# Performance work log

Measured on AMD Instinct MI355X. Metric: run time of the kernel, lower is better.

## Reference

```python
import jax, jax.numpy as jnp
import numpy as np

EMBED = 1024
N_HEAD = 16
D_HID = EMBED // N_HEAD
R_FF = 4
D_FF = EMBED * R_FF
LN_EPS = 1e-5


def layer_norm(x, gamma, beta):
    mu = jnp.mean(x, axis=-1, keepdims=True)
    var = jnp.var(x, axis=-1, keepdims=True)
    return (x - mu) * jax.lax.rsqrt(var + LN_EPS) * gamma + beta


def setup_inputs() -> dict:
    key = jax.random.key(0)
    ks = jax.random.split(key, 10)
    B, S = 4, 2048
    # torch nn.Linear stores weight as [out, in]; y = x @ W.T
    def xavier(k, shape):
        fan_out, fan_in = shape
        lim = np.sqrt(6.0 / (fan_in + fan_out))
        return jax.random.uniform(k, shape, jnp.float32, -lim, lim)
    return {
        "x": jax.random.normal(ks[0], (B, S, EMBED), jnp.float32),
        "Wq": xavier(ks[1], (EMBED, EMBED)),
        "Wk": xavier(ks[2], (EMBED, EMBED)),
        "Wv": xavier(ks[3], (EMBED, EMBED)),
        "Wo": xavier(ks[4], (EMBED, EMBED)),
        "bo": jnp.zeros((EMBED,), jnp.float32),
        "ln1_g": jnp.ones((EMBED,), jnp.float32),
        "ln1_b": jnp.zeros((EMBED,), jnp.float32),
        "ln2_g": jnp.ones((EMBED,), jnp.float32),
        "ln2_b": jnp.zeros((EMBED,), jnp.float32),
        "W1": jax.random.normal(ks[5], (D_FF, EMBED), jnp.float32) * np.sqrt(2.0 / EMBED),
        "b1": jnp.zeros((D_FF,), jnp.float32),
        "W2": xavier(ks[6], (EMBED, D_FF)),
        "b2": jnp.zeros((EMBED,), jnp.float32),
    }


def reference(x, Wq, Wk, Wv, Wo, bo, ln1_g, ln1_b, ln2_g, ln2_b, W1, b1, W2, b2):
    B, S, E = x.shape
    scaling = 1.0 / np.sqrt(D_HID)
    # --- attention (pre-LN), dropout = identity (eval) ---
    xn = layer_norm(x, ln1_g, ln1_b)
    q = (xn @ Wq.T).reshape(B, S, N_HEAD, D_HID) * scaling
    k = (xn @ Wk.T).reshape(B, S, N_HEAD, D_HID)
    v = (xn @ Wv.T).reshape(B, S, N_HEAD, D_HID)
    scores = jnp.einsum("bqhd,bkhd->bhqk", q, k)
    attn = jax.nn.softmax(scores, axis=-1)
    out = jnp.einsum("bhqk,bkhd->bqhd", attn, v).reshape(B, S, E)
    out = out @ Wo.T + bo
    x = x + out
    # --- feed-forward (pre-LN) ---
    xn = layer_norm(x, ln2_g, ln2_b)
    h = jax.nn.relu(xn @ W1.T + b1)
    x = x + (h @ W2.T + b2)
    return x
```

## Files before the change

kernel.cpp:

```cpp
#include <hip/hip_runtime.h>
#include <hip/hip_bf16.h>
#include <cstdint>


typedef __attribute__((ext_vector_type(8))) short bf16x8;
typedef __attribute__((ext_vector_type(4))) float f32x4;

#define LDSAS __attribute__((address_space(3)))
#define GLBAS __attribute__((address_space(1)))

#define CQK 0.18033688011112044f

union APU { unsigned u[4]; bf16x8 v; };

__device__ __forceinline__ unsigned short f2bf(float f) {
  union { float f; unsigned u; } c; c.f = f;
  unsigned u = c.u + 0x7fffu + ((c.u >> 16) & 1u);
  return (unsigned short)(u >> 16);
}

__device__ __forceinline__ unsigned pk2(float a, float b) {
  __hip_bfloat162 h = __float22bfloat162_rn(make_float2(a, b));
  union { __hip_bfloat162 h; unsigned u; } c; c.h = h; return c.u;
}

__device__ __forceinline__ void async16(const unsigned short* g, unsigned short* l) {
  __builtin_amdgcn_global_load_lds((const GLBAS unsigned int*)g,
                                   (LDSAS unsigned int*)l, 16, 0, 0);
}

__global__ void cvt_all(const float* __restrict__ q, const float* __restrict__ k,
                        const float* __restrict__ v, const float* __restrict__ o,
                        const float* __restrict__ w1, const float* __restrict__ w2,
                        unsigned short* __restrict__ wsb) {
  const long i = (long)blockIdx.x * 256 + threadIdx.x;
  const float* src; unsigned short* dst; long off;
  if (i < 1048576) {
    const long seg = i >> 18, o4 = i & 262143;
    src = (seg == 0) ? q : (seg == 1) ? k : (seg == 2) ? v : o;
    dst = wsb + ((seg == 3) ? 3145728L : seg * 1048576L);
    off = o4;
  } else if (i < 2097152) {
    src = w1; dst = wsb + 4194304; off = i - 1048576;
  } else {
    src = w2; dst = wsb + 8388608; off = i - 2097152;
  }
  const float4 vv = ((const float4*)src)[off];
  ushort4 r;
  r.x = f2bf(vv.x); r.y = f2bf(vv.y); r.z = f2bf(vv.z); r.w = f2bf(vv.w);
  ((ushort4*)dst)[off] = r;
}

__global__ void ln_fwd(const float* __restrict__ x, const float* __restrict__ g,
                       const float* __restrict__ bb, unsigned short* __restrict__ outp) {
  const int row = blockIdx.x, tid = threadIdx.x;
  const float4 v = ((const float4*)(x + (long)row * 1024))[tid];
  float s  = v.x + v.y + v.z + v.w;
  float sq = v.x * v.x + v.y * v.y + v.z * v.z + v.w * v.w;
#pragma unroll
  for (int off = 1; off < 64; off <<= 1) {
    s  += __shfl_xor(s, off);
    sq += __shfl_xor(sq, off);
  }
  __shared__ float red[8];
  const int wv = tid >> 6, lane = tid & 63;
  if (lane == 0) { red[wv] = s; red[4 + wv] = sq; }
  __syncthreads();
  s  = red[0] + red[1] + red[2] + red[3];
  sq = red[4] + red[5] + red[6] + red[7];
  const float mu  = s * (1.f / 1024.f);
  const float var = sq * (1.f / 1024.f) - mu * mu;
  const float rstd = rsqrtf(var + 1e-5f);
  const float4 gv = ((const float4*)g)[tid];
  const float4 bv = ((const float4*)bb)[tid];
  ushort4 o;
  o.x = f2bf((v.x - mu) * rstd * gv.x + bv.x);
  o.y = f2bf((v.y - mu) * rstd * gv.y + bv.y);
  o.z = f2bf((v.z - mu) * rstd * gv.z + bv.z);
  o.w = f2bf((v.w - mu) * rstd * gv.w + bv.w);
  ((ushort4*)(outp + (long)row * 1024))[tid] = o;
}

template <int EPI>
__launch_bounds__(256, 3)
__global__ void gemm_bt(const unsigned short* __restrict__ A,
                        const unsigned short* __restrict__ B,
                        void* __restrict__ Cout,
                        const float* __restrict__ bias,
                        const float* __restrict__ res,
                        unsigned short* __restrict__ vt4,
                        int M, int N, int K) {
  __shared__ __align__(16) unsigned short As[128 * 64];
  __shared__ __align__(16) unsigned short Bs[128 * 64];
  const int tid  = threadIdx.x;
  const int lane = tid & 63;
  const int wvu  = __builtin_amdgcn_readfirstlane(tid >> 6);
  const int quad = lane >> 4, l16 = lane & 15;
  const int wm = wvu >> 1, wn = wvu & 1;

  const int gx = gridDim.x;
  const int id = blockIdx.y * gx + blockIdx.x;
  const int xcd = id & 7, slot = id >> 3;
  const int by = xcd * 8 + (slot & 7);
  const int bx = slot >> 3;
  const long m0 = (long)by * 128, n0 = (long)bx * 128;

  f32x4 acc[4][4];
#pragma unroll
  for (int i = 0; i < 4; i++)
#pragma unroll
    for (int j = 0; j < 4; j++) acc[i][j] = (f32x4){0.f, 0.f, 0.f, 0.f};

  const int rxA = l16 & 7;
  const int c0A = quad ^ rxA;
  int srow[4], sgc[4];
#pragma unroll
  for (int j = 0; j < 4; ++j) {
    const int s = wvu * 256 + j * 64 + lane;
    srow[j] = s >> 3;
    sgc[j] = ((s & 7) ^ (srow[j] & 7)) * 8;
  }

  for (int k0 = 0; k0 < K; k0 += 64) {
    __syncthreads();
#pragma unroll
    for (int j = 0; j < 4; ++j) {
      const int db = (wvu * 256 + j * 64) * 8;
      async16(A + (m0 + srow[j]) * K + k0 + sgc[j], As + db);
      async16(B + (n0 + srow[j]) * K + k0 + sgc[j], Bs + db);
    }
    __syncthreads();

#pragma unroll
    for (int kc = 0; kc < 2; ++kc) {
      const int ch = (c0A ^ (kc * 4)) * 8;
      bf16x8 af[4], bfr[4];
#pragma unroll
      for (int t = 0; t < 4; ++t) {
        af[t]  = *(const bf16x8*)(As + (wm * 64 + t * 16 + l16) * 64 + ch);
        bfr[t] = *(const bf16x8*)(Bs + (wn * 64 + t * 16 + l16) * 64 + ch);
      }
#pragma unroll
      for (int mt = 0; mt < 4; ++mt)
#pragma unroll
        for (int nt = 0; nt < 4; ++nt)
          acc[mt][nt] = __builtin_amdgcn_mfma_f32_16x16x32_bf16(af[mt], bfr[nt],
                                                                acc[mt][nt], 0, 0, 0);
    }
  }

  if (EPI == 3) {
#pragma unroll
    for (int nt = 0; nt < 4; ++nt) {
      const long col = n0 + wn * 64 + nt * 16 + l16;
      if (col < 2048) {
        const float scl = (col < 1024) ? CQK : 1.0f;
#pragma unroll
        for (int mt = 0; mt < 4; ++mt)
#pragma unroll
          for (int r = 0; r < 4; ++r) {
            const long row = m0 + wm * 64 + mt * 16 + quad * 4 + r;
            ((unsigned short*)Cout)[row * (long)N + col] = f2bf(acc[mt][nt][r] * scl);
          }
      } else {
        const int hd = (int)(col - 2048);
        const int h = hd >> 6, d = hd & 63;
#pragma unroll
        for (int mt = 0; mt < 4; ++mt) {
          const long row = m0 + wm * 64 + mt * 16 + quad * 4;
          const int b_ = (int)(row >> 11);
          const int kv = (int)(row & 2047);
          const int t_ = kv >> 6;
          const int sk = kv & 63;
          const int kvp4 = (sk & 32) | ((sk & 16) >> 2) | ((sk & 8) << 1) | ((sk & 4) << 1);
          const int kk = kvp4 >> 3, half = (kvp4 >> 2) & 1;
          const int cc = d * 8 + ((kk + d) & 7);
          const int u = cc * 2 + half;
          ushort4 o;
          o.x = f2bf(acc[mt][nt][0]);
          o.y = f2bf(acc[mt][nt][1]);
          o.z = f2bf(acc[mt][nt][2]);
          o.w = f2bf(acc[mt][nt][3]);
          *(ushort4*)(vt4 + ((long)((b_ * 16 + h) * 32 + t_)) * 4096 + u * 4) = o;
        }
      }
    }
  } else {
#pragma unroll
    for (int nt = 0; nt < 4; ++nt) {
      const long col = n0 + wn * 64 + nt * 16 + l16;
      float bv = 0.f;
      if (EPI == 1 || EPI == 2) bv = bias[col];
#pragma unroll
      for (int mt = 0; mt < 4; ++mt) {
#pragma unroll
        for (int r = 0; r < 4; ++r) {
          const long row = m0 + wm * 64 + mt * 16 + quad * 4 + r;
          const long idx = row * (long)N + col;
          float v = acc[mt][nt][r];
          if (EPI == 0) {
            ((unsigned short*)Cout)[idx] = f2bf(v);
          } else if (EPI == 1) {
            ((float*)Cout)[idx] = v + bv + res[idx];
          } else {
            v += bv;
            ((unsigned short*)Cout)[idx] = f2bf(v > 0.f ? v : 0.f);
          }
        }
      }
    }
  }
}

#define W2_LDA(AF, BUF, H)                                                      \
  do {                                                                          \
    const unsigned short* _p = As + ((BUF) * 2 + (H)) * 4096;                   \
    _Pragma("unroll") for (int _m = 0; _m < 2; ++_m) {                          \
      AF[_m][0] = *(const bf16x8*)(_p + (_m * 32 + rA) * 64 + chk0);            \
      AF[_m][1] = *(const bf16x8*)(_p + (_m * 32 + rA) * 64 + chk1);            \
    }                                                                           \
  } while (0)

#define W2_LDB(BF, BUF, H)                                                      \
  do {                                                                          \
    const unsigned short* _p = Bs + ((BUF) * 2 + (H)) * 8192;                   \
    _Pragma("unroll") for (int _n = 0; _n < 2; ++_n) {                          \
      BF[_n][0] = *(const bf16x8*)(_p + (_n * 64 + rB) * 64 + chk0);            \
      BF[_n][1] = *(const bf16x8*)(_p + (_n * 64 + rB) * 64 + chk1);            \
    }                                                                           \
  } while (0)

#define W2_MFMA(AH, BH, AF, BF)                                                 \
  do {                                                                          \
    _Pragma("unroll") for (int _m = 0; _m < 2; ++_m)                            \
    _Pragma("unroll") for (int _n = 0; _n < 2; ++_n) {                          \
      acc[(AH) * 2 + _m][(BH) * 2 + _n] =                                       \
          __builtin_amdgcn_mfma_f32_16x16x32_bf16(                              \
              AF[_m][0], BF[_n][0], acc[(AH) * 2 + _m][(BH) * 2 + _n], 0, 0, 0);\
      acc[(AH) * 2 + _m][(BH) * 2 + _n] =                                       \
          __builtin_amdgcn_mfma_f32_16x16x32_bf16(                              \
              AF[_m][1], BF[_n][1], acc[(AH) * 2 + _m][(BH) * 2 + _n], 0, 0, 0);\
    }                                                                           \
  } while (0)

#define PH_MID()                                                                \
  __builtin_amdgcn_s_barrier();                                                 \
  asm volatile("s_waitcnt lgkmcnt(0)" ::: "memory");                            \
  __builtin_amdgcn_sched_barrier(0);                                            \
  __builtin_amdgcn_s_setprio(1)

#define PH_END()                                                                \
  __builtin_amdgcn_s_setprio(0);                                                \
  __builtin_amdgcn_sched_barrier(0);                                            \
  __builtin_amdgcn_s_barrier();                                                 \
  __builtin_amdgcn_sched_barrier(0)

__launch_bounds__(512, 2)
__global__ void gemm_w2(const unsigned short* __restrict__ A,
                        const unsigned short* __restrict__ B,
                        float* __restrict__ Cout,
                        const float* __restrict__ bias,
                        const float* __restrict__ res,
                        int M, int N, int K) {
  extern __shared__ __align__(16) unsigned short lds[];
  unsigned short* As = lds;
  unsigned short* Bs = lds + 16384;

  const int tid  = threadIdx.x;
  const int lane = tid & 63;
  const int wv   = __builtin_amdgcn_readfirstlane(tid >> 6);
  const int quad = lane >> 4, l16 = lane & 15;
  const int wm = wv >> 2, wn = wv & 3;

  const int id = blockIdx.x;
  const int xcd = id & 7, slot = id >> 3;
  const int by = xcd * 8 + (slot & 7);
  const int bx = slot >> 3;
  const long m0 = (long)by * 128, n0 = (long)bx * 256;

  const int s0 = wv * 64 + lane;
  const int r0 = s0 >> 3;
  const int c0 = (s0 ^ r0) & 7;
  const int s1 = 512 + s0;
  const int r1 = s1 >> 3;
  const int c1 = (s1 ^ r1) & 7;
  const long rt0 = (long)r0 * K + c0 * 8;
  const long rt1 = (long)r1 * K + c1 * 8;
  const unsigned short* Ab = A + m0 * K;
  const unsigned short* Bb = B + n0 * K;

  const int rA = wm * 16 + l16;
  const int rB = wn * 16 + l16;
  const int chk0 = (quad ^ (l16 & 7)) * 8;
  const int chk1 = chk0 ^ 32;

  f32x4 acc[4][4];
#pragma unroll
  for (int a_ = 0; a_ < 4; ++a_)
#pragma unroll
    for (int b_ = 0; b_ < 4; ++b_) acc[a_][b_] = (f32x4){0.f, 0.f, 0.f, 0.f};

  auto stgA = [&](int b, int h, long kk) {
    const unsigned short* s = Ab + (long)h * 64 * K + kk;
    async16(s + rt0, As + (b * 2 + h) * 4096 + wv * 512);
  };
  auto stgB = [&](int b, int h, long kk) {
    const unsigned short* s = Bb + (long)h * 128 * K + kk;
    unsigned short* d = Bs + (b * 2 + h) * 8192 + wv * 512;
    async16(s + rt0, d);
    async16(s + rt1, d + 4096);
  };

  stgA(0, 0, 0); stgB(0, 1, 0); stgA(0, 1, 0); stgB(0, 0, 0);
  stgA(1, 0, 64); stgB(1, 1, 64); stgA(1, 1, 64);
  asm volatile("s_waitcnt vmcnt(4)" ::: "memory");
  __builtin_amdgcn_s_barrier();
  __builtin_amdgcn_sched_barrier(0);

  const int NI = K >> 7;
  for (int it = 0; it < NI; ++it) {
    const long kt  = (long)it * 128;
    const long ku  = kt + 64;
    const long kt2 = kt + 128;
    const long kt3 = kt + 192;
    const bool more = (it + 1 < NI);

    {
      bf16x8 a0[2][2], a1[2][2], b0[2][2], b1[2][2];
      W2_LDA(a0, 0, 0); W2_LDB(b0, 0, 0);
      stgB(1, 0, ku);
      PH_MID();
      W2_MFMA(0, 0, a0, b0);
      PH_END();
      W2_LDB(b1, 0, 1);
      if (more) stgA(0, 0, kt2);
      PH_MID();
      W2_MFMA(0, 1, a0, b1);
      PH_END();
      W2_LDA(a1, 0, 1);
      if (more) stgB(0, 1, kt2);
      PH_MID();
      W2_MFMA(1, 1, a1, b1);
      PH_END();
      W2_LDB(b0, 0, 0);
      if (more) stgA(0, 1, kt2);
      PH_MID();
      W2_MFMA(1, 0, a1, b0);
      __builtin_amdgcn_s_setprio(0);
      __builtin_amdgcn_sched_barrier(0);
      if (more) { asm volatile("s_waitcnt vmcnt(4)" ::: "memory"); }
      else      { asm volatile("s_waitcnt vmcnt(0)" ::: "memory"); }
      __builtin_amdgcn_s_barrier();
      __builtin_amdgcn_sched_barrier(0);
    }
    {
      bf16x8 a0[2][2], a1[2][2], b0[2][2], b1[2][2];
      W2_LDA(a0, 1, 0); W2_LDB(b0, 1, 0);
      if (more) stgB(0, 0, kt2);
      PH_MID();
      W2_MFMA(0, 0, a0, b0);
      PH_END();
      W2_LDB(b1, 1, 1);
      if (more) stgA(1, 0, kt3);
      PH_MID();
      W2_MFMA(0, 1, a0, b1);
      PH_END();
      W2_LDA(a1, 1, 1);
      if (more) stgB(1, 1, kt3);
      PH_MID();
      W2_MFMA(1, 1, a1, b1);
      PH_END();
      W2_LDB(b0, 1, 0);
      if (more) stgA(1, 1, kt3);
      PH_MID();
      W2_MFMA(1, 0, a1, b0);
      __builtin_amdgcn_s_setprio(0);
      __builtin_amdgcn_sched_barrier(0);
      if (more) { asm volatile("s_waitcnt vmcnt(4)" ::: "memory"); }
      __builtin_amdgcn_s_barrier();
      __builtin_amdgcn_sched_barrier(0);
    }
  }

#pragma unroll
  for (int nt = 0; nt < 4; ++nt) {
    const long col = n0 + nt * 64 + wn * 16 + l16;
    const float bv = bias[col];
#pragma unroll
    for (int mt = 0; mt < 4; ++mt) {
#pragma unroll
      for (int r = 0; r < 4; ++r) {
        const long row = m0 + mt * 32 + wm * 16 + quad * 4 + r;
        const long idx = row * (long)N + col;
        Cout[idx] = acc[mt][nt][r] + bv + res[idx];
      }
    }
  }
}

__launch_bounds__(256, 4)
__global__ void attn_fwd(const unsigned short* __restrict__ qkv,
                         const unsigned short* __restrict__ vt,
                         unsigned short* __restrict__ outp) {
  __shared__ __align__(16) unsigned short lds[20480];

  const int tid = threadIdx.x;
  const int lane = tid & 63;
  const int wv = __builtin_amdgcn_readfirstlane(tid >> 6);
  const int quad = lane >> 4, l16 = lane & 15;

  const int id = blockIdx.y * 16 + blockIdx.x;
  const int xcd = id & 7, slot = id >> 3;
  const int bh = xcd * 8 + (slot >> 4);
  const int qt = slot & 15;
  const int b = bh >> 4, h = bh & 15;
  const long rowbase = (long)b * 2048;
  const int hoff = h * 64;

  const int rot0 = (quad + l16) & 7;
  const int rot1 = rot0 ^ 4;

  bf16x8 bq[2][2];
#pragma unroll
  for (int s = 0; s < 2; ++s) {
    const long qrow = rowbase + qt * 128 + wv * 32 + s * 16 + l16;
    const unsigned short* qp = qkv + qrow * 3072 + hoff;
    bq[s][0] = *(const bf16x8*)(qp + quad * 8);
    bq[s][1] = *(const bf16x8*)(qp + (quad ^ 4) * 8);
  }
  __builtin_amdgcn_sched_barrier(0);

  const int c0 = wv * 64 + lane;
  const int r0 = c0 >> 3;
  const int ks = ((c0 & 7) - r0) & 7;
  const unsigned short* kptr = qkv + (rowbase + r0) * 3072 + 1024 + hoff + ks * 8;
  const unsigned short* vptr = vt + (long)bh * 131072 + (long)c0 * 8;

  auto stage = [&](int t) {
    unsigned short* kdst = lds + ((t & 1) << 12) + wv * 512;
    unsigned short* vdst = lds + 8192 + ((t % 3) << 12) + wv * 512;
    const unsigned short* kp = kptr + (long)t * 64 * 3072;
    const unsigned short* vp = vptr + (long)t * 4096;
#pragma unroll
    for (int j = 0; j < 2; ++j) {
      async16(kp + (long)j * 32 * 3072, kdst + j * 2048);
      async16(vp + j * 2048, vdst + j * 2048);
    }
  };

  bf16x8 ones;
#pragma unroll
  for (int i = 0; i < 8; ++i) ones[i] = (short)0x3F80;

  f32x4 oacc[2][4], lacc[2];
#pragma unroll
  for (int s = 0; s < 2; ++s) {
    lacc[s] = (f32x4){0.f, 0.f, 0.f, 0.f};
#pragma unroll
    for (int i = 0; i < 4; ++i) oacc[s][i] = (f32x4){0.f, 0.f, 0.f, 0.f};
  }

  auto QK = [&](int t, f32x4 (&sx)[2][4]) {
    const unsigned short* Kb = lds + ((t & 1) << 12);
    __builtin_amdgcn_s_setprio(1);
#pragma unroll
    for (int tt = 0; tt < 4; ++tt) {
      const int ar = tt * 16 + l16;
      bf16x8 ak0 = *(const bf16x8*)(Kb + ar * 64 + rot0 * 8);
      bf16x8 ak1 = *(const bf16x8*)(Kb + ar * 64 + rot1 * 8);
#pragma unroll
      for (int s = 0; s < 2; ++s) {
        f32x4 z = (f32x4){0.f, 0.f, 0.f, 0.f};
        z = __builtin_amdgcn_mfma_f32_16x16x32_bf16(ak0, bq[s][0], z, 0, 0, 0);
        sx[s][tt] = __builtin_amdgcn_mfma_f32_16x16x32_bf16(ak1, bq[s][1], z, 0, 0, 0);
      }
    }
    __builtin_amdgcn_s_setprio(0);
  };

  auto SM = [&](f32x4 (&sx)[2][4], APU (&ap)[2][2]) {
#pragma unroll
    for (int s = 0; s < 2; ++s)
#pragma unroll
      for (int hf = 0; hf < 2; ++hf) {
#pragma unroll
        for (int tt = 0; tt < 2; ++tt) {
          const f32x4 sv = sx[s][hf * 2 + tt];
          const float p0 = __builtin_amdgcn_exp2f(sv[0]);
          const float p1 = __builtin_amdgcn_exp2f(sv[1]);
          const float p2 = __builtin_amdgcn_exp2f(sv[2]);
          const float p3 = __builtin_amdgcn_exp2f(sv[3]);
          ap[s][hf].u[tt * 2 + 0] = pk2(p0, p1);
          ap[s][hf].u[tt * 2 + 1] = pk2(p2, p3);
        }
        lacc[s] = __builtin_amdgcn_mfma_f32_16x16x32_bf16(ap[s][hf].v, ones,
                                                          lacc[s], 0, 0, 0);
      }
  };

  auto PV = [&](int t, APU (&ap)[2][2]) {
    const unsigned short* Vb = lds + 8192 + ((t % 3) << 12);
    __builtin_amdgcn_s_setprio(1);
#pragma unroll
    for (int hf = 0; hf < 2; ++hf) {
      const int vbase = (hf ? rot1 : rot0) * 8;
#pragma unroll
      for (int dt = 0; dt < 4; ++dt) {
        bf16x8 bv = *(const bf16x8*)(Vb + vbase + (dt * 16 + l16) * 64);
#pragma unroll
        for (int s = 0; s < 2; ++s)
          oacc[s][dt] = __builtin_amdgcn_mfma_f32_16x16x32_bf16(ap[s][hf].v, bv,
                                                                oacc[s][dt], 0, 0, 0);
      }
    }
    __builtin_amdgcn_s_setprio(0);
  };

  auto body = [&](int kt, f32x4 (&scur)[2][4], f32x4 (&snxt)[2][4], bool qknext) {
    const bool more = (kt + 2 < 32);
    if (more) stage(kt + 2);
    APU ap[2][2];
    SM(scur, ap);
    if (more) { asm volatile("s_waitcnt vmcnt(4)" ::: "memory"); }
    else      { asm volatile("s_waitcnt vmcnt(0)" ::: "memory"); }
    __builtin_amdgcn_s_barrier();
    __builtin_amdgcn_sched_barrier(0);
    PV(kt, ap);
    if (qknext) QK(kt + 1, snxt);
    __builtin_amdgcn_s_barrier();
    __builtin_amdgcn_sched_barrier(0);
  };

  stage(0); stage(1);
  asm volatile("s_waitcnt vmcnt(4)" ::: "memory");
  __builtin_amdgcn_s_barrier();
  __builtin_amdgcn_sched_barrier(0);

  f32x4 sacc0[2][4], sacc1[2][4];
  QK(0, sacc0);
  __builtin_amdgcn_s_barrier();
  __builtin_amdgcn_sched_barrier(0);

  for (int it = 0; it < 16; ++it) {
    body(2 * it,     sacc0, sacc1, true);
    body(2 * it + 1, sacc1, sacc0, it < 15);
  }

#pragma unroll
  for (int s = 0; s < 2; ++s) {
    float linv[4];
#pragma unroll
    for (int r = 0; r < 4; ++r) linv[r] = 1.f / lacc[s][r];
#pragma unroll
    for (int dt = 0; dt < 4; ++dt)
#pragma unroll
      for (int r = 0; r < 4; ++r) {
        const long row = rowbase + qt * 128 + wv * 32 + s * 16 + quad * 4 + r;
        outp[row * 1024 + hoff + dt * 16 + l16] = f2bf(oacc[s][dt][r] * linv[r]);
      }
  }
}

extern "C" void kernel_launch(void* const* d_in, const int* in_sizes, int n_in,
                              void* d_out, int out_size, void* d_ws, size_t ws_size,
                              hipStream_t stream) {
  (void)in_sizes; (void)n_in; (void)out_size; (void)ws_size;
  const float* x   = (const float*)d_in[0];
  const float* Wq  = (const float*)d_in[1];
  const float* Wk  = (const float*)d_in[2];
  const float* Wv  = (const float*)d_in[3];
  const float* Wo  = (const float*)d_in[4];
  const float* bo  = (const float*)d_in[5];
  const float* g1  = (const float*)d_in[6];
  const float* be1 = (const float*)d_in[7];
  const float* g2  = (const float*)d_in[8];
  const float* be2 = (const float*)d_in[9];
  const float* W1  = (const float*)d_in[10];
  const float* bf1 = (const float*)d_in[11];
  const float* W2  = (const float*)d_in[12];
  const float* bf2 = (const float*)d_in[13];

  static bool s_attr = false;
  if (!s_attr) {
    hipFuncSetAttribute(reinterpret_cast<const void*>(&gemm_w2),
                        hipFuncAttributeMaxDynamicSharedMemorySize, 98304);
    s_attr = true;
  }

  char* ws = (char*)d_ws;
  unsigned short* wqkv  = (unsigned short*)(ws);
  unsigned short* wo    = (unsigned short*)(ws + 6291456);
  unsigned short* w1    = (unsigned short*)(ws + 8388608);
  unsigned short* w2    = (unsigned short*)(ws + 16777216);
  unsigned short* xn    = (unsigned short*)(ws + 25165824);
  unsigned short* big   = (unsigned short*)(ws + 41943040);
  unsigned short* vtg   = (unsigned short*)(ws + 92274688);
  unsigned short* attnb = (unsigned short*)(ws + 109051904);
  float*          x1    = (float*)(ws + 125829120);

  cvt_all<<<12288, 256, 0, stream>>>(Wq, Wk, Wv, Wo, W1, W2, wqkv);

  ln_fwd<<<8192, 256, 0, stream>>>(x, g1, be1, xn);
  gemm_bt<3><<<dim3(24, 64), 256, 0, stream>>>(xn, wqkv, big, nullptr, nullptr,
                                               vtg, 8192, 3072, 1024);
  attn_fwd<<<dim3(16, 64), 256, 0, stream>>>(big, vtg, attnb);
  gemm_bt<1><<<dim3(8, 64), 256, 0, stream>>>(attnb, wo, x1, bo, x,
                                              nullptr, 8192, 1024, 1024);
  ln_fwd<<<8192, 256, 0, stream>>>(x1, g2, be2, xn);
  gemm_bt<2><<<dim3(32, 64), 256, 0, stream>>>(xn, w1, big, bf1, nullptr,
                                               nullptr, 8192, 4096, 1024);
  gemm_w2<<<dim3(256), 512, 98304, stream>>>(big, w2, (float*)d_out, bf2, x1,
                                             8192, 1024, 4096);
}
```

Measured before the change: 449.7 us.

## Halve attention tiles to 64 queries and 32 keys, re-layout V transpose

The attention kernel now processes 64 query rows per block (16 per wave) and 32-key tiles instead of 128 queries and 64 keys. LDS use is halved and launch bounds are raised to 8 blocks per CU, and the grid doubles. The QKV GEMM epilogue writes V in a new swizzled 32-key tile layout that matches the new PV read pattern. The aim is higher occupancy and more blocks for latency hiding. In exchange, K/V reuse per block drops, so global/L2 traffic doubles, and each tile has a larger share of barriers and loop overhead.

Result: no change. 453.2 us (+0.8%).

```diff
diff --git a/kernel.cpp b/kernel.cpp
--- a/kernel.cpp
+++ b/kernel.cpp
@@ -165,23 +165,22 @@
       } else {
         const int hd = (int)(col - 2048);
         const int h = hd >> 6, d = hd & 63;
+        const int dsw = d + (d >> 2);
 #pragma unroll
         for (int mt = 0; mt < 4; ++mt) {
           const long row = m0 + wm * 64 + mt * 16 + quad * 4;
           const int b_ = (int)(row >> 11);
           const int kv = (int)(row & 2047);
-          const int t_ = kv >> 6;
-          const int sk = kv & 63;
-          const int kvp4 = (sk & 32) | ((sk & 16) >> 2) | ((sk & 8) << 1) | ((sk & 4) << 1);
-          const int kk = kvp4 >> 3, half = (kvp4 >> 2) & 1;
-          const int cc = d * 8 + ((kk + d) & 7);
-          const int u = cc * 2 + half;
+          const int t32 = kv >> 5;
+          const int q_ = (kv >> 2) & 3;
+          const int tt = (kv >> 4) & 1;
+          const int c = d * 4 + ((q_ + dsw) & 3);
           ushort4 o;
           o.x = f2bf(acc[mt][nt][0]);
           o.y = f2bf(acc[mt][nt][1]);
           o.z = f2bf(acc[mt][nt][2]);
           o.w = f2bf(acc[mt][nt][3]);
-          *(ushort4*)(vt4 + ((long)((b_ * 16 + h) * 32 + t_)) * 4096 + u * 4) = o;
+          *(ushort4*)(vt4 + ((long)((b_ * 16 + h) * 64 + t32)) * 2048 + c * 8 + tt * 4) = o;
         }
       }
     }
@@ -398,21 +397,21 @@
   }
 }
 
-__launch_bounds__(256, 4)
+__launch_bounds__(256, 8)
 __global__ void attn_fwd(const unsigned short* __restrict__ qkv,
                          const unsigned short* __restrict__ vt,
                          unsigned short* __restrict__ outp) {
-  __shared__ __align__(16) unsigned short lds[20480];
+  __shared__ __align__(16) unsigned short lds[10240];
 
   const int tid = threadIdx.x;
   const int lane = tid & 63;
   const int wv = __builtin_amdgcn_readfirstlane(tid >> 6);
   const int quad = lane >> 4, l16 = lane & 15;
 
-  const int id = blockIdx.y * 16 + blockIdx.x;
+  const int id = blockIdx.y * 32 + blockIdx.x;
   const int xcd = id & 7, slot = id >> 3;
-  const int bh = xcd * 8 + (slot >> 4);
-  const int qt = slot & 15;
+  const int bh = xcd * 8 + (slot >> 5);
+  const int qt = slot & 31;
   const int b = bh >> 4, h = bh & 15;
   const long rowbase = (long)b * 2048;
   const int hoff = h * 64;
@@ -420,13 +419,12 @@
   const int rot0 = (quad + l16) & 7;
   const int rot1 = rot0 ^ 4;
 
-  bf16x8 bq[2][2];
-#pragma unroll
-  for (int s = 0; s < 2; ++s) {
-    const long qrow = rowbase + qt * 128 + wv * 32 + s * 16 + l16;
+  bf16x8 bq0, bq1;
+  {
+    const long qrow = rowbase + qt * 64 + wv * 16 + l16;
     const unsigned short* qp = qkv + qrow * 3072 + hoff;
-    bq[s][0] = *(const bf16x8*)(qp + quad * 8);
-    bq[s][1] = *(const bf16x8*)(qp + (quad ^ 4) * 8);
+    bq0 = *(const bf16x8*)(qp + quad * 8);
+    bq1 = *(const bf16x8*)(qp + (quad ^ 4) * 8);
   }
   __builtin_amdgcn_sched_barrier(0);
 
@@ -437,91 +435,69 @@
   const unsigned short* vptr = vt + (long)bh * 131072 + (long)c0 * 8;
 
   auto stage = [&](int t) {
-    unsigned short* kdst = lds + ((t & 1) << 12) + wv * 512;
-    unsigned short* vdst = lds + 8192 + ((t % 3) << 12) + wv * 512;
-    const unsigned short* kp = kptr + (long)t * 64 * 3072;
-    const unsigned short* vp = vptr + (long)t * 4096;
-#pragma unroll
-    for (int j = 0; j < 2; ++j) {
-      async16(kp + (long)j * 32 * 3072, kdst + j * 2048);
-      async16(vp + j * 2048, vdst + j * 2048);
-    }
+    unsigned short* kdst = lds + ((t & 1) << 11) + wv * 512;
+    unsigned short* vdst = lds + 4096 + ((t % 3) << 11) + wv * 512;
+    async16(kptr + (long)t * 32 * 3072, kdst);
+    async16(vptr + (long)t * 2048, vdst);
   };
 
   bf16x8 ones;
 #pragma unroll
   for (int i = 0; i < 8; ++i) ones[i] = (short)0x3F80;
 
-  f32x4 oacc[2][4], lacc[2];
-#pragma unroll
-  for (int s = 0; s < 2; ++s) {
-    lacc[s] = (f32x4){0.f, 0.f, 0.f, 0.f};
-#pragma unroll
-    for (int i = 0; i < 4; ++i) oacc[s][i] = (f32x4){0.f, 0.f, 0.f, 0.f};
-  }
-
-  auto QK = [&](int t, f32x4 (&sx)[2][4]) {
-    const unsigned short* Kb = lds + ((t & 1) << 12);
+  f32x4 oacc[4], lacc;
+  lacc = (f32x4){0.f, 0.f, 0.f, 0.f};
+#pragma unroll
+  for (int i = 0; i < 4; ++i) oacc[i] = (f32x4){0.f, 0.f, 0.f, 0.f};
+
+  auto QK = [&](int t, f32x4 (&sx)[2]) {
+    const unsigned short* Kb = lds + ((t & 1) << 11);
     __builtin_amdgcn_s_setprio(1);
 #pragma unroll
-    for (int tt = 0; tt < 4; ++tt) {
+    for (int tt = 0; tt < 2; ++tt) {
       const int ar = tt * 16 + l16;
       bf16x8 ak0 = *(const bf16x8*)(Kb + ar * 64 + rot0 * 8);
       bf16x8 ak1 = *(const bf16x8*)(Kb + ar * 64 + rot1 * 8);
-#pragma unroll
-      for (int s = 0; s < 2; ++s) {
-        f32x4 z = (f32x4){0.f, 0.f, 0.f, 0.f};
-        z = __builtin_amdgcn_mfma_f32_16x16x32_bf16(ak0, bq[s][0], z, 0, 0, 0);
-        sx[s][tt] = __builtin_amdgcn_mfma_f32_16x16x32_bf16(ak1, bq[s][1], z, 0, 0, 0);
-      }
+      f32x4 z = (f32x4){0.f, 0.f, 0.f, 0.f};
+      z = __builtin_amdgcn_mfma_f32_16x16x32_bf16(ak0, bq0, z, 0, 0, 0);
+      sx[tt] = __builtin_amdgcn_mfma_f32_16x16x32_bf16(ak1, bq1, z, 0, 0, 0);
     }
     __builtin_amdgcn_s_setprio(0);
   };
 
-  auto SM = [&](f32x4 (&sx)[2][4], APU (&ap)[2][2]) {
-#pragma unroll
-    for (int s = 0; s < 2; ++s)
-#pragma unroll
-      for (int hf = 0; hf < 2; ++hf) {
-#pragma unroll
-        for (int tt = 0; tt < 2; ++tt) {
-          const f32x4 sv = sx[s][hf * 2 + tt];
-          const float p0 = __builtin_amdgcn_exp2f(sv[0]);
-          const float p1 = __builtin_amdgcn_exp2f(sv[1]);
-          const float p2 = __builtin_amdgcn_exp2f(sv[2]);
-          const float p3 = __builtin_amdgcn_exp2f(sv[3]);
-          ap[s][hf].u[tt * 2 + 0] = pk2(p0, p1);
-          ap[s][hf].u[tt * 2 + 1] = pk2(p2, p3);
-        }
-        lacc[s] = __builtin_amdgcn_mfma_f32_16x16x32_bf16(ap[s][hf].v, ones,
-                                                          lacc[s], 0, 0, 0);
-      }
-  };
-
-  auto PV = [&](int t, APU (&ap)[2][2]) {
-    const unsigned short* Vb = lds + 8192 + ((t % 3) << 12);
+  auto SM = [&](f32x4 (&sx)[2], APU& ap) {
+#pragma unroll
+    for (int tt = 0; tt < 2; ++tt) {
+      const f32x4 sv = sx[tt];
+      const float p0 = __builtin_amdgcn_exp2f(sv[0]);
+      const float p1 = __builtin_amdgcn_exp2f(sv[1]);
+      const float p2 = __builtin_amdgcn_exp2f(sv[2]);
+      const float p3 = __builtin_amdgcn_exp2f(sv[3]);
+      ap.u[tt * 2 + 0] = pk2(p0, p1);
+      ap.u[tt * 2 + 1] = pk2(p2, p3);
+    }
+    lacc = __builtin_amdgcn_mfma_f32_16x16x32_bf16(ap.v, ones, lacc, 0, 0, 0);
+  };
+
+  auto PV = [&](int t, APU& ap) {
+    const unsigned short* Vb = lds + 4096 + ((t % 3) << 11);
     __builtin_amdgcn_s_setprio(1);
 #pragma unroll
-    for (int hf = 0; hf < 2; ++hf) {
-      const int vbase = (hf ? rot1 : rot0) * 8;
-#pragma unroll
-      for (int dt = 0; dt < 4; ++dt) {
-        bf16x8 bv = *(const bf16x8*)(Vb + vbase + (dt * 16 + l16) * 64);
-#pragma unroll
-        for (int s = 0; s < 2; ++s)
-          oacc[s][dt] = __builtin_amdgcn_mfma_f32_16x16x32_bf16(ap[s][hf].v, bv,
-                                                                oacc[s][dt], 0, 0, 0);
-      }
+    for (int dt = 0; dt < 4; ++dt) {
+      const int d = dt * 16 + l16;
+      const int rotv = (quad + d + (d >> 2)) & 3;
+      bf16x8 bv = *(const bf16x8*)(Vb + d * 32 + rotv * 8);
+      oacc[dt] = __builtin_amdgcn_mfma_f32_16x16x32_bf16(ap.v, bv, oacc[dt], 0, 0, 0);
     }
     __builtin_amdgcn_s_setprio(0);
   };
 
-  auto body = [&](int kt, f32x4 (&scur)[2][4], f32x4 (&snxt)[2][4], bool qknext) {
-    const bool more = (kt + 2 < 32);
+  auto body = [&](int kt, f32x4 (&scur)[2], f32x4 (&snxt)[2], bool qknext) {
+    const bool more = (kt + 2 < 64);
     if (more) stage(kt + 2);
-    APU ap[2][2];
+    APU ap;
     SM(scur, ap);
-    if (more) { asm volatile("s_waitcnt vmcnt(4)" ::: "memory"); }
+    if (more) { asm volatile("s_waitcnt vmcnt(2)" ::: "memory"); }
     else      { asm volatile("s_waitcnt vmcnt(0)" ::: "memory"); }
     __builtin_amdgcn_s_barrier();
     __builtin_amdgcn_sched_barrier(0);
@@ -532,33 +508,30 @@
   };
 
   stage(0); stage(1);
-  asm volatile("s_waitcnt vmcnt(4)" ::: "memory");
+  asm volatile("s_waitcnt vmcnt(2)" ::: "memory");
   __builtin_amdgcn_s_barrier();
   __builtin_amdgcn_sched_barrier(0);
 
-  f32x4 sacc0[2][4], sacc1[2][4];
+  f32x4 sacc0[2], sacc1[2];
   QK(0, sacc0);
   __builtin_amdgcn_s_barrier();
   __builtin_amdgcn_sched_barrier(0);
 
-  for (int it = 0; it < 16; ++it) {
+  for (int it = 0; it < 32; ++it) {
     body(2 * it,     sacc0, sacc1, true);
-    body(2 * it + 1, sacc1, sacc0, it < 15);
-  }
-
-#pragma unroll
-  for (int s = 0; s < 2; ++s) {
-    float linv[4];
-#pragma unroll
-    for (int r = 0; r < 4; ++r) linv[r] = 1.f / lacc[s][r];
-#pragma unroll
-    for (int dt = 0; dt < 4; ++dt)
-#pragma unroll
-      for (int r = 0; r < 4; ++r) {
-        const long row = rowbase + qt * 128 + wv * 32 + s * 16 + quad * 4 + r;
-        outp[row * 1024 + hoff + dt * 16 + l16] = f2bf(oacc[s][dt][r] * linv[r]);
-      }
-  }
+    body(2 * it + 1, sacc1, sacc0, it < 31);
+  }
+
+  float linv[4];
+#pragma unroll
+  for (int r = 0; r < 4; ++r) linv[r] = 1.f / lacc[r];
+#pragma unroll
+  for (int dt = 0; dt < 4; ++dt)
+#pragma unroll
+    for (int r = 0; r < 4; ++r) {
+      const long row = rowbase + qt * 64 + wv * 16 + quad * 4 + r;
+      outp[row * 1024 + hoff + dt * 16 + l16] = f2bf(oacc[dt][r] * linv[r]);
+    }
 }
 
 extern "C" void kernel_launch(void* const* d_in, const int* in_sizes, int n_in,
@@ -603,7 +576,7 @@
   ln_fwd<<<8192, 256, 0, stream>>>(x, g1, be1, xn);
   gemm_bt<3><<<dim3(24, 64), 256, 0, stream>>>(xn, wqkv, big, nullptr, nullptr,
                                                vtg, 8192, 3072, 1024);
-  attn_fwd<<<dim3(16, 64), 256, 0, stream>>>(big, vtg, attnb);
+  attn_fwd<<<dim3(32, 64), 256, 0, stream>>>(big, vtg, attnb);
   gemm_bt<1><<<dim3(8, 64), 256, 0, stream>>>(attnb, wo, x1, bo, x,
                                               nullptr, 8192, 1024, 1024);
   ln_fwd<<<8192, 256, 0, stream>>>(x1, g2, be2, xn);
```
